# Optimization experiments

Measured on AMD Instinct MI355X. Metric: run time of the kernel, lower is better.

Reference implementation:

```python
import jax, jax.numpy as jnp
import numpy as np

DIM = 1024
NUM_HEADS = 16
NUM_KV_HEADS = 2
HEAD_DIM = DIM // NUM_HEADS          # 64
REPEATS = NUM_HEADS // NUM_KV_HEADS  # 8
WINDOW = 256
HALF = WINDOW // 2                   # 128
BATCH, SEQ = 2, 2048


def setup_inputs() -> dict:
    key = jax.random.key(0)
    ks = jax.random.split(key, 9)
    sc = 1.0 / np.sqrt(DIM)
    return {
        "x":  jax.random.normal(ks[0], (BATCH, SEQ, DIM), jnp.float32),
        "Wq": jax.random.normal(ks[1], (DIM, NUM_HEADS * HEAD_DIM), jnp.float32) * sc,
        "bq": jax.random.normal(ks[2], (NUM_HEADS * HEAD_DIM,), jnp.float32) * 0.01,
        "Wk": jax.random.normal(ks[3], (DIM, NUM_KV_HEADS * HEAD_DIM), jnp.float32) * sc,
        "bk": jax.random.normal(ks[4], (NUM_KV_HEADS * HEAD_DIM,), jnp.float32) * 0.01,
        "Wv": jax.random.normal(ks[5], (DIM, NUM_KV_HEADS * HEAD_DIM), jnp.float32) * sc,
        "bv": jax.random.normal(ks[6], (NUM_KV_HEADS * HEAD_DIM,), jnp.float32) * 0.01,
        "Wo": jax.random.normal(ks[7], (DIM, DIM), jnp.float32) * sc,
        "bo": jax.random.normal(ks[8], (DIM,), jnp.float32) * 0.01,
    }


def reference(x, Wq, bq, Wk, bk, Wv, bv, Wo, bo):
    # Training-path GQA sliding-window attention (faithful to the torch module):
    #  - K/V zero-padded by HALF on each side of the sequence; window of size
    #    WINDOW centered on each query position (unfold with step 1).
    #  - NOTE (faithful): the original code builds mask = tril(ones)[-1], which is
    #    an all-ones row, so masked_fill is a no-op -> NO causal mask inside the
    #    window; padded positions contribute score 0 (not -inf) to the softmax.
    #  - NOTE (faithful): the training path does NOT scale scores by 1/sqrt(d).
    b, s, _ = x.shape
    q = (x @ Wq + bq).reshape(b, s, NUM_HEADS, HEAD_DIM).transpose(0, 2, 1, 3)      # [b,H,s,d]
    k = (x @ Wk + bk).reshape(b, s, NUM_KV_HEADS, HEAD_DIM).transpose(0, 2, 1, 3)   # [b,G,s,d]
    v = (x @ Wv + bv).reshape(b, s, NUM_KV_HEADS, HEAD_DIM).transpose(0, 2, 1, 3)

    kp = jnp.pad(k, ((0, 0), (0, 0), (HALF, HALF), (0, 0)))  # [b,G,s+W,d]
    vp = jnp.pad(v, ((0, 0), (0, 0), (HALF, HALF), (0, 0)))

    # window gather indices: window i covers padded positions [i, i+W)
    idx = jnp.arange(s)[:, None] + jnp.arange(WINDOW)[None, :]  # [s,W]
    k_win = kp[:, :, idx]  # [b,G,s,W,d]  (gather at kv-head granularity, not H)
    v_win = vp[:, :, idx]

    # group query heads by kv head: head h -> kv group h // REPEATS
    qg = q.reshape(b, NUM_KV_HEADS, REPEATS, s, HEAD_DIM)        # [b,G,r,s,d]
    scores = jnp.einsum('bgrsd,bgswd->bgrsw', qg, k_win)         # no scaling (faithful)
    probs = jax.nn.softmax(scores, axis=-1)
    out = jnp.einsum('bgrsw,bgswd->bgrsd', probs, v_win)         # [b,G,r,s,d]

    out = out.reshape(b, NUM_HEADS, s, HEAD_DIM).transpose(0, 2, 1, 3).reshape(b, s, DIM)
    return out @ Wo + bo
```

## Files before the change

kernel.cpp:

```cpp
#include <hip/hip_runtime.h>
#include <hip/hip_fp16.h>

typedef _Float16 h16;
typedef __attribute__((ext_vector_type(4))) _Float16 h16x4;
typedef __attribute__((ext_vector_type(8))) _Float16 h16x8;
typedef __attribute__((ext_vector_type(4))) float f32x4;

#define DIM   1024
#define SEQ   2048
#define NKV   2
#define HD    64
#define HALFW 128
#define NQKV  1280
#define KSTG  288
#define KCOLS 272
#define VSTR  312
#define LOG2E 1.4426950408889634f

__global__ void preprocess_kernel(const float* __restrict__ x,
                                  const float* __restrict__ bq,
                                  const float* __restrict__ bk,
                                  const float* __restrict__ bv,
                                  const float* __restrict__ Wq,
                                  const float* __restrict__ Wk,
                                  const float* __restrict__ Wv,
                                  const float* __restrict__ Wo,
                                  h16* __restrict__ xh, float* __restrict__ bqkv,
                                  h16* __restrict__ wqkvt, h16* __restrict__ wot)
{
    __shared__ float tile[32][33];
    const int tid = threadIdx.x;
    const int blk = blockIdx.x;
    if (blk < 2048) {
        int i = blk * 256 + tid;
        size_t base = (size_t)i * 8;
        float4 a = *(const float4*)(x + base);
        float4 b = *(const float4*)(x + base + 4);
        h16x8 o = { (h16)a.x,(h16)a.y,(h16)a.z,(h16)a.w,
                    (h16)b.x,(h16)b.y,(h16)b.z,(h16)b.w };
        *(h16x8*)(xh + base) = o;
        if (i < NQKV) {
            float v = (i < DIM) ? bq[i] * LOG2E
                                : (i < DIM+128 ? bk[i-DIM] : bv[i-DIM-128]);
            bqkv[i] = v;
        }
        return;
    }
    const int tx = tid & 31, ty = tid >> 5;
    if (blk < 2048 + 1280) {
        int bid = blk - 2048;
        int n0 = (bid % 40) * 32, k0 = (bid / 40) * 32;
        const float* src; int ldn, noff; float scl;
        if (n0 < DIM)          { src = Wq; ldn = DIM; noff = n0; scl = LOG2E; }
        else if (n0 < DIM+128) { src = Wk; ldn = 128; noff = n0 - DIM; scl = 1.f; }
        else                   { src = Wv; ldn = 128; noff = n0 - DIM - 128; scl = 1.f; }
#pragma unroll
        for (int i = 0; i < 4; ++i)
            tile[ty + 8*i][tx] = src[(size_t)(k0 + ty + 8*i)*ldn + noff + tx] * scl;
        __syncthreads();
#pragma unroll
        for (int i = 0; i < 4; ++i)
            wqkvt[(size_t)(n0 + ty + 8*i)*DIM + k0 + tx] = (h16)tile[tx][ty + 8*i];
    } else {
        int bid = blk - 3328;
        int n0 = (bid % 32) * 32, k0 = (bid / 32) * 32;
#pragma unroll
        for (int i = 0; i < 4; ++i)
            tile[ty + 8*i][tx] = Wo[(size_t)(k0 + ty + 8*i)*DIM + n0 + tx];
        __syncthreads();
#pragma unroll
        for (int i = 0; i < 4; ++i)
            wot[(size_t)(n0 + ty + 8*i)*DIM + k0 + tx] = (h16)tile[tx][ty + 8*i];
    }
}

__global__ void vtrans_kernel(const h16* __restrict__ v, h16* __restrict__ vt)
{
    __shared__ h16 tile[32][33];
    const int s0 = blockIdx.x * 32, d0 = blockIdx.y * 32, bg = blockIdx.z;
    const h16* src = v  + (size_t)bg * SEQ * HD;
    h16*       dst = vt + (size_t)bg * SEQ * HD;
    const int tx = threadIdx.x & 31, ty = threadIdx.x >> 5;
#pragma unroll
    for (int i = 0; i < 4; ++i)
        tile[ty + 8*i][tx] = src[(size_t)(s0 + ty + 8*i)*HD + d0 + tx];
    __syncthreads();
#pragma unroll
    for (int i = 0; i < 4; ++i)
        dst[(size_t)(d0 + ty + 8*i)*SEQ + s0 + tx] = tile[tx][ty + 8*i];
}

template<int MODE>
__global__ __launch_bounds__(256, 3)
void gemm_kernel(const h16* __restrict__ A, const h16* __restrict__ Bt,
                 const float* __restrict__ bias,
                 h16* __restrict__ qo, h16* __restrict__ ko, h16* __restrict__ vo,
                 float* __restrict__ co, int K, int nx)
{
    __shared__ __align__(16) h16 As[2][128*64];
    __shared__ __align__(16) h16 Bs[2][64*64];
    const int nwg = gridDim.x, bid = blockIdx.x;
    const int wg = (bid & 7) * (nwg >> 3) + (bid >> 3);
    const int m0 = (wg / nx) * 128, n0 = (wg % nx) * 64;
    const int tid = threadIdx.x, lane = tid & 63, wid = tid >> 6;
    const int wr = wid >> 1, wc = wid & 1;
    f32x4 acc[4][2] = {};

    auto stage = [&](int buf, int kk) {
#pragma unroll
        for (int i = 0; i < 4; ++i) {
            int slot = i*256 + tid;
            int row = slot >> 3;
            int scol = ((slot & 7) ^ (row & 7)) * 8;
            __builtin_amdgcn_global_load_lds(
                (const __attribute__((address_space(1))) void*)(A + (size_t)(m0 + row)*K + kk + scol),
                (__attribute__((address_space(3))) void*)(&As[buf][slot*8]), 16, 0, 0);
        }
#pragma unroll
        for (int i = 0; i < 2; ++i) {
            int slot = i*256 + tid;
            int row = slot >> 3;
            int scol = ((slot & 7) ^ (row & 7)) * 8;
            __builtin_amdgcn_global_load_lds(
                (const __attribute__((address_space(1))) void*)(Bt + (size_t)(n0 + row)*K + kk + scol),
                (__attribute__((address_space(3))) void*)(&Bs[buf][slot*8]), 16, 0, 0);
        }
    };
    auto compute = [&](int buf) {
#pragma unroll
        for (int k2 = 0; k2 < 2; ++k2) {
            h16x8 a[4], b[2];
#pragma unroll
            for (int mi = 0; mi < 4; ++mi) {
                int row = wr*64 + mi*16 + (lane & 15);
                int cc = (k2*4 + (lane >> 4)) ^ (row & 7);
                a[mi] = *(const h16x8*)(&As[buf][row*64 + cc*8]);
            }
#pragma unroll
            for (int ni = 0; ni < 2; ++ni) {
                int row = wc*32 + ni*16 + (lane & 15);
                int cc = (k2*4 + (lane >> 4)) ^ (row & 7);
                b[ni] = *(const h16x8*)(&Bs[buf][row*64 + cc*8]);
            }
#pragma unroll
            for (int mi = 0; mi < 4; ++mi)
#pragma unroll
                for (int ni = 0; ni < 2; ++ni)
                    acc[mi][ni] = __builtin_amdgcn_mfma_f32_16x16x32_f16(a[mi], b[ni], acc[mi][ni], 0, 0, 0);
        }
    };

    const int ns = K >> 6;
    stage(0, 0);
    int cur = 0;
    for (int i = 0; i < ns; ++i) {
        if (i < ns-1) {
            stage(cur ^ 1, (i+1) << 6);
            asm volatile("s_waitcnt vmcnt(6)" ::: "memory");
        } else {
            asm volatile("s_waitcnt vmcnt(0)" ::: "memory");
        }
        __builtin_amdgcn_s_barrier();
        __builtin_amdgcn_sched_barrier(0);
        compute(cur);
        if (i < ns-1) {
            __builtin_amdgcn_s_barrier();
            __builtin_amdgcn_sched_barrier(0);
        }
        cur ^= 1;
    }

#pragma unroll
    for (int ni = 0; ni < 2; ++ni) {
        int n = n0 + wc*32 + ni*16 + (lane & 15);
        float bv = bias[n];
#pragma unroll
        for (int mi = 0; mi < 4; ++mi) {
            int mb = m0 + wr*64 + mi*16 + (lane >> 4)*4;
#pragma unroll
            for (int r = 0; r < 4; ++r) {
                int m = mb + r;
                float v = acc[mi][ni][r] + bv;
                if (MODE == 1) {
                    co[(size_t)m*DIM + n] = v;
                } else {
                    h16 hv = (h16)v;
                    if (n < DIM) {
                        qo[(size_t)m*DIM + n] = hv;
                    } else {
                        int nn = n - DIM;
                        int bi2 = m >> 11, s = m & 2047;
                        int g = (nn & 127) >> 6, d = nn & 63;
                        h16* dstp = (nn < 128) ? ko : vo;
                        dstp[(((size_t)(bi2*NKV + g))*SEQ + s)*HD + d] = hv;
                    }
                }
            }
        }
    }
}

__global__ __launch_bounds__(512)
void attn_kernel(const h16* __restrict__ qb, const h16* __restrict__ kb,
                 const h16* __restrict__ vtb, h16* __restrict__ ob)
{
    extern __shared__ char smem[];
    h16* Ks  = (h16*)smem;
    h16* Vts = (h16*)(smem + 36864);
    h16* Ps  = (h16*)(smem + 36864 + 39936);
    const int tid = threadIdx.x, lane = tid & 63, wid = tid >> 6;
    const int qt = blockIdx.x, g = blockIdx.y, bi = blockIdx.z;
    const int s0 = qt * 32;
    const size_t kvbase = ((size_t)(bi*NKV + g)) * SEQ * HD;

    for (int slot = tid; slot < KSTG*8; slot += 512) {
        int row = slot >> 3, cc = slot & 7;
        int kpos = s0 - HALFW + row;
        h16x8 val = {0,0,0,0,0,0,0,0};
        if (kpos >= 0 && kpos < SEQ)
            val = *(const h16x8*)(kb + kvbase + (size_t)kpos*HD + cc*8);
        *(h16x8*)(Ks + row*64 + ((cc ^ (row & 7)) * 8)) = val;
    }
    for (int slot = tid; slot < 64*38; slot += 512) {
        int row = slot / 38, cc = slot - row*38;
        int c0 = cc * 8;
        int kp0 = s0 - HALFW + c0;
        const h16* vrow = vtb + kvbase + (size_t)row*SEQ;
        h16x8 val = {0,0,0,0,0,0,0,0};
        if (kp0 >= 0 && kp0 + 8 <= SEQ) {
            val = *(const h16x8*)(vrow + kp0);
        } else {
#pragma unroll
            for (int j = 0; j < 8; ++j) {
                int kp = kp0 + j;
                val[j] = (kp >= 0 && kp < SEQ) ? vrow[kp] : (h16)0;
            }
        }
        *(h16x8*)(Vts + row*VSTR + c0) = val;
    }
    h16* P = Ps + wid * 16 * VSTR;
    for (int i = lane; i < 256; i += 64)
        P[(i >> 4)*VSTR + KCOLS + (i & 15)] = (h16)0;
    __syncthreads();

    const int h = g*8 + wid;
    const int colbase = lane & 15;
    const int rowbase = (lane >> 4) * 4;
    const int kg = rowbase;

    for (int strip = 0; strip < 2; ++strip) {
        const int ss0 = s0 + strip*16;
        h16x8 aq[2];
#pragma unroll
        for (int c = 0; c < 2; ++c)
            aq[c] = *(const h16x8*)(qb + ((size_t)(bi*SEQ + ss0 + colbase))*DIM
                                    + h*HD + c*32 + (lane >> 4)*8);

        f32x4 sc[17];
        __builtin_amdgcn_s_setprio(1);
#pragma unroll
        for (int t = 0; t < 17; ++t) {
            f32x4 z = {0.f,0.f,0.f,0.f};
#pragma unroll
            for (int c = 0; c < 2; ++c) {
                int key = strip*16 + t*16 + colbase;
                h16x8 kf = *(const h16x8*)(Ks + key*64 + (((c*4 + (lane >> 4)) ^ (key & 7)) * 8));
                z = __builtin_amdgcn_mfma_f32_16x16x32_f16(kf, aq[c], z, 0, 0, 0);
            }
            sc[t] = z;
        }
        __builtin_amdgcn_s_setprio(0);

        float mx = -1e30f;
#pragma unroll
        for (int r = 0; r < 4; ++r) {
            float v0  = (kg + r >= colbase) ? sc[0][r]  : -1e30f;
            float v16 = (kg + r <  colbase) ? sc[16][r] : -1e30f;
            sc[0][r] = v0; sc[16][r] = v16;
            mx = fmaxf(mx, fmaxf(v0, v16));
        }
#pragma unroll
        for (int t = 1; t < 16; ++t)
#pragma unroll
            for (int r = 0; r < 4; ++r) mx = fmaxf(mx, sc[t][r]);
        mx = fmaxf(mx, __shfl_xor(mx, 16));
        mx = fmaxf(mx, __shfl_xor(mx, 32));
        float sum = 0.f;
#pragma unroll
        for (int t = 0; t < 17; ++t)
#pragma unroll
            for (int r = 0; r < 4; ++r) {
                float p = exp2f(sc[t][r] - mx);
                sc[t][r] = p;
                sum += p;
            }
        sum += __shfl_xor(sum, 16);
        sum += __shfl_xor(sum, 32);
        float inv = 1.0f / sum;

#pragma unroll
        for (int t = 0; t < 17; ++t) {
            h16x4 pk = { (h16)(sc[t][0]*inv), (h16)(sc[t][1]*inv),
                         (h16)(sc[t][2]*inv), (h16)(sc[t][3]*inv) };
            *(h16x4*)(P + colbase*VSTR + t*16 + kg) = pk;
        }

        f32x4 ao[4] = {};
        __builtin_amdgcn_s_setprio(1);
#pragma unroll
        for (int c = 0; c < 9; ++c) {
            h16x8 pa = *(const h16x8*)(P + colbase*VSTR + c*32 + (lane >> 4)*8);
            int vcol = strip*16 + c*32 + (lane >> 4)*8;
#pragma unroll
            for (int t2 = 0; t2 < 4; ++t2) {
                h16x8 vb = *(const h16x8*)(Vts + (t2*16 + colbase)*VSTR + vcol);
                ao[t2] = __builtin_amdgcn_mfma_f32_16x16x32_f16(pa, vb, ao[t2], 0, 0, 0);
            }
        }
        __builtin_amdgcn_s_setprio(0);
#pragma unroll
        for (int t2 = 0; t2 < 4; ++t2)
#pragma unroll
            for (int r = 0; r < 4; ++r)
                ob[((size_t)(bi*SEQ + ss0 + rowbase + r))*DIM + h*HD + t2*16 + colbase]
                    = (h16)ao[t2][r];
        if (strip == 0) __syncthreads();
    }
}

extern "C" void kernel_launch(void* const* d_in, const int* in_sizes, int n_in,
                              void* d_out, int out_size, void* d_ws, size_t ws_size,
                              hipStream_t stream)
{
    const float* x  = (const float*)d_in[0];
    const float* Wq = (const float*)d_in[1];
    const float* bq = (const float*)d_in[2];
    const float* Wk = (const float*)d_in[3];
    const float* bk = (const float*)d_in[4];
    const float* Wv = (const float*)d_in[5];
    const float* bv = (const float*)d_in[6];
    const float* Wo = (const float*)d_in[7];
    const float* bo = (const float*)d_in[8];
    float* out = (float*)d_out;
    char* ws = (char*)d_ws;

    h16*   xh    = (h16*)(ws);
    h16*   wqkvt = (h16*)(ws + 8388608);
    h16*   wot   = (h16*)(ws + 11010048);
    float* bqkv  = (float*)(ws + 13107200);
    h16*   q_b   = (h16*)(ws + 13112320);
    h16*   k_b   = (h16*)(ws + 21500928);
    h16*   vt_b  = (h16*)(ws + 22549504);
    h16*   att_b = (h16*)(ws + 23598080);
    h16*   v_b   = att_b;

    preprocess_kernel<<<4352, 256, 0, stream>>>(x, bq, bk, bv, Wq, Wk, Wv, Wo,
                                                xh, bqkv, wqkvt, wot);
    gemm_kernel<0><<<640, 256, 0, stream>>>(xh, wqkvt, bqkv,
                                            q_b, k_b, v_b, nullptr, DIM, 20);
    vtrans_kernel<<<dim3(64, 2, 4), 256, 0, stream>>>(v_b, vt_b);
    hipFuncSetAttribute((const void*)attn_kernel,
                        hipFuncAttributeMaxDynamicSharedMemorySize, 156672);
    attn_kernel<<<dim3(64,2,2), 512, 156672, stream>>>(q_b, k_b, vt_b, att_b);
    gemm_kernel<1><<<512, 256, 0, stream>>>(att_b, wot, bo,
                                            nullptr, nullptr, nullptr, out, DIM, 16);
}
```

Measured before the change: 68.37 us.

## Read K/V directly from zero-padded global buffers instead of staging in LDS

K and transposed V are written into global buffers padded by HALF zero rows/columns on each side, with the padding zeroed by extra preprocess blocks. The attention kernel then drops LDS staging of K/V and the block-wide barrier, and loads MFMA operands straight from global/L2, keeping only the per-wave P tile in shared memory. Blocks shrink to 256 threads (4 heads each) with a 4-blocks-per-CU launch bound, for more occupancy and less LDS. The cost is that the 8 heads sharing a KV group (now split across two blocks) each issue their own global loads, which depend on cache hits.

After: 92.01 us. 1.35x slower.

```diff
diff --git a/kernel.cpp b/kernel.cpp
--- a/kernel.cpp
+++ b/kernel.cpp
@@ -12,9 +12,9 @@
 #define HD    64
 #define HALFW 128
 #define NQKV  1280
-#define KSTG  288
-#define KCOLS 272
-#define VSTR  312
+#define SPAD  2304
+#define KPS   (SPAD*HD)
+#define PSTR  296
 #define LOG2E 1.4426950408889634f
 
 __global__ void preprocess_kernel(const float* __restrict__ x,
@@ -26,7 +26,8 @@
                                   const float* __restrict__ Wv,
                                   const float* __restrict__ Wo,
                                   h16* __restrict__ xh, float* __restrict__ bqkv,
-                                  h16* __restrict__ wqkvt, h16* __restrict__ wot)
+                                  h16* __restrict__ wqkvt, h16* __restrict__ wot,
+                                  h16* __restrict__ kpad, h16* __restrict__ vtpad)
 {
     __shared__ float tile[32][33];
     const int tid = threadIdx.x;
@@ -46,6 +47,22 @@
         }
         return;
     }
+    if (blk >= 4352) {
+        int idx = (blk - 4352) * 256 + tid;
+        h16x8 z8 = {};
+        if (idx < 8192) {
+            int bg = idx >> 11, j = idx & 2047;
+            size_t off = (j < 1024) ? (size_t)j*8 : (size_t)2176*HD + (size_t)(j-1024)*8;
+            *(h16x8*)(kpad + (size_t)bg*KPS + off) = z8;
+        } else {
+            int i2 = idx - 8192;
+            int bg = i2 >> 11, j = i2 & 2047;
+            int d = j >> 5, r = j & 31;
+            size_t off = (size_t)d*SPAD + ((r & 16) ? 2176 : 0) + (size_t)(r & 15)*8;
+            *(h16x8*)(vtpad + (size_t)bg*KPS + off) = z8;
+        }
+        return;
+    }
     const int tx = tid & 31, ty = tid >> 5;
     if (blk < 2048 + 1280) {
         int bid = blk - 2048;
@@ -79,7 +96,7 @@
     __shared__ h16 tile[32][33];
     const int s0 = blockIdx.x * 32, d0 = blockIdx.y * 32, bg = blockIdx.z;
     const h16* src = v  + (size_t)bg * SEQ * HD;
-    h16*       dst = vt + (size_t)bg * SEQ * HD;
+    h16*       dst = vt + (size_t)bg * KPS;
     const int tx = threadIdx.x & 31, ty = threadIdx.x >> 5;
 #pragma unroll
     for (int i = 0; i < 4; ++i)
@@ -87,7 +104,7 @@
     __syncthreads();
 #pragma unroll
     for (int i = 0; i < 4; ++i)
-        dst[(size_t)(d0 + ty + 8*i)*SEQ + s0 + tx] = tile[tx][ty + 8*i];
+        dst[(size_t)(d0 + ty + 8*i)*SPAD + HALFW + s0 + tx] = tile[tx][ty + 8*i];
 }
 
 template<int MODE>
@@ -191,8 +208,10 @@
                         int nn = n - DIM;
                         int bi2 = m >> 11, s = m & 2047;
                         int g = (nn & 127) >> 6, d = nn & 63;
-                        h16* dstp = (nn < 128) ? ko : vo;
-                        dstp[(((size_t)(bi2*NKV + g))*SEQ + s)*HD + d] = hv;
+                        if (nn < 128)
+                            ko[((size_t)(bi2*NKV + g)*SPAD + s + HALFW)*HD + d] = hv;
+                        else
+                            vo[(((size_t)(bi2*NKV + g))*SEQ + s)*HD + d] = hv;
                     }
                 }
             }
@@ -200,61 +219,31 @@
     }
 }
 
-__global__ __launch_bounds__(512)
-void attn_kernel(const h16* __restrict__ qb, const h16* __restrict__ kb,
-                 const h16* __restrict__ vtb, h16* __restrict__ ob)
-{
-    extern __shared__ char smem[];
-    h16* Ks  = (h16*)smem;
-    h16* Vts = (h16*)(smem + 36864);
-    h16* Ps  = (h16*)(smem + 36864 + 39936);
+__global__ __launch_bounds__(256, 4)
+void attn_kernel(const h16* __restrict__ qb, const h16* __restrict__ kpad,
+                 const h16* __restrict__ vtpad, h16* __restrict__ ob)
+{
+    __shared__ h16 Ps[4][16][PSTR];
     const int tid = threadIdx.x, lane = tid & 63, wid = tid >> 6;
-    const int qt = blockIdx.x, g = blockIdx.y, bi = blockIdx.z;
+    const int qt = blockIdx.x, quad = blockIdx.y, bi = blockIdx.z;
+    const int g = quad >> 1, h = quad*4 + wid;
     const int s0 = qt * 32;
-    const size_t kvbase = ((size_t)(bi*NKV + g)) * SEQ * HD;
-
-    for (int slot = tid; slot < KSTG*8; slot += 512) {
-        int row = slot >> 3, cc = slot & 7;
-        int kpos = s0 - HALFW + row;
-        h16x8 val = {0,0,0,0,0,0,0,0};
-        if (kpos >= 0 && kpos < SEQ)
-            val = *(const h16x8*)(kb + kvbase + (size_t)kpos*HD + cc*8);
-        *(h16x8*)(Ks + row*64 + ((cc ^ (row & 7)) * 8)) = val;
-    }
-    for (int slot = tid; slot < 64*38; slot += 512) {
-        int row = slot / 38, cc = slot - row*38;
-        int c0 = cc * 8;
-        int kp0 = s0 - HALFW + c0;
-        const h16* vrow = vtb + kvbase + (size_t)row*SEQ;
-        h16x8 val = {0,0,0,0,0,0,0,0};
-        if (kp0 >= 0 && kp0 + 8 <= SEQ) {
-            val = *(const h16x8*)(vrow + kp0);
-        } else {
-#pragma unroll
-            for (int j = 0; j < 8; ++j) {
-                int kp = kp0 + j;
-                val[j] = (kp >= 0 && kp < SEQ) ? vrow[kp] : (h16)0;
-            }
-        }
-        *(h16x8*)(Vts + row*VSTR + c0) = val;
-    }
-    h16* P = Ps + wid * 16 * VSTR;
+    const int q = lane & 15, hi = lane >> 4;
+    const int rowbase = hi * 4;
+    const h16* Kb = kpad  + (size_t)(bi*NKV + g)*KPS + (size_t)s0*HD;
+    const h16* Vb = vtpad + (size_t)(bi*NKV + g)*KPS + s0;
+    h16* P = &Ps[wid][0][0];
+
     for (int i = lane; i < 256; i += 64)
-        P[(i >> 4)*VSTR + KCOLS + (i & 15)] = (h16)0;
-    __syncthreads();
-
-    const int h = g*8 + wid;
-    const int colbase = lane & 15;
-    const int rowbase = (lane >> 4) * 4;
-    const int kg = rowbase;
+        P[(i >> 4)*PSTR + 272 + (i & 15)] = (h16)0;
 
     for (int strip = 0; strip < 2; ++strip) {
         const int ss0 = s0 + strip*16;
         h16x8 aq[2];
 #pragma unroll
         for (int c = 0; c < 2; ++c)
-            aq[c] = *(const h16x8*)(qb + ((size_t)(bi*SEQ + ss0 + colbase))*DIM
-                                    + h*HD + c*32 + (lane >> 4)*8);
+            aq[c] = *(const h16x8*)(qb + ((size_t)(bi*SEQ + ss0 + q))*DIM
+                                    + h*HD + c*32 + hi*8);
 
         f32x4 sc[17];
         __builtin_amdgcn_s_setprio(1);
@@ -263,8 +252,8 @@
             f32x4 z = {0.f,0.f,0.f,0.f};
 #pragma unroll
             for (int c = 0; c < 2; ++c) {
-                int key = strip*16 + t*16 + colbase;
-                h16x8 kf = *(const h16x8*)(Ks + key*64 + (((c*4 + (lane >> 4)) ^ (key & 7)) * 8));
+                h16x8 kf = *(const h16x8*)(Kb + (size_t)(strip*16 + t*16 + q)*HD
+                                           + (c*4 + hi)*8);
                 z = __builtin_amdgcn_mfma_f32_16x16x32_f16(kf, aq[c], z, 0, 0, 0);
             }
             sc[t] = z;
@@ -274,8 +263,8 @@
         float mx = -1e30f;
 #pragma unroll
         for (int r = 0; r < 4; ++r) {
-            float v0  = (kg + r >= colbase) ? sc[0][r]  : -1e30f;
-            float v16 = (kg + r <  colbase) ? sc[16][r] : -1e30f;
+            float v0  = (rowbase + r >= q) ? sc[0][r]  : -1e30f;
+            float v16 = (rowbase + r <  q) ? sc[16][r] : -1e30f;
             sc[0][r] = v0; sc[16][r] = v16;
             mx = fmaxf(mx, fmaxf(v0, v16));
         }
@@ -302,18 +291,18 @@
         for (int t = 0; t < 17; ++t) {
             h16x4 pk = { (h16)(sc[t][0]*inv), (h16)(sc[t][1]*inv),
                          (h16)(sc[t][2]*inv), (h16)(sc[t][3]*inv) };
-            *(h16x4*)(P + colbase*VSTR + t*16 + kg) = pk;
+            *(h16x4*)(P + q*PSTR + t*16 + rowbase) = pk;
         }
 
         f32x4 ao[4] = {};
         __builtin_amdgcn_s_setprio(1);
 #pragma unroll
         for (int c = 0; c < 9; ++c) {
-            h16x8 pa = *(const h16x8*)(P + colbase*VSTR + c*32 + (lane >> 4)*8);
-            int vcol = strip*16 + c*32 + (lane >> 4)*8;
+            h16x8 pa = *(const h16x8*)(P + q*PSTR + c*32 + hi*8);
+            int vcol = strip*16 + c*32 + hi*8;
 #pragma unroll
             for (int t2 = 0; t2 < 4; ++t2) {
-                h16x8 vb = *(const h16x8*)(Vts + (t2*16 + colbase)*VSTR + vcol);
+                h16x8 vb = *(const h16x8*)(Vb + (size_t)(t2*16 + q)*SPAD + vcol);
                 ao[t2] = __builtin_amdgcn_mfma_f32_16x16x32_f16(pa, vb, ao[t2], 0, 0, 0);
             }
         }
@@ -322,9 +311,8 @@
         for (int t2 = 0; t2 < 4; ++t2)
 #pragma unroll
             for (int r = 0; r < 4; ++r)
-                ob[((size_t)(bi*SEQ + ss0 + rowbase + r))*DIM + h*HD + t2*16 + colbase]
+                ob[((size_t)(bi*SEQ + ss0 + rowbase + r))*DIM + h*HD + t2*16 + q]
                     = (h16)ao[t2][r];
-        if (strip == 0) __syncthreads();
     }
 }
 
@@ -349,19 +337,17 @@
     h16*   wot   = (h16*)(ws + 11010048);
     float* bqkv  = (float*)(ws + 13107200);
     h16*   q_b   = (h16*)(ws + 13112320);
-    h16*   k_b   = (h16*)(ws + 21500928);
-    h16*   vt_b  = (h16*)(ws + 22549504);
-    h16*   att_b = (h16*)(ws + 23598080);
+    h16*   k_pad = (h16*)(ws + 21500928);
+    h16*   vt_pad= (h16*)(ws + 22680576);
+    h16*   att_b = (h16*)(ws + 23860224);
     h16*   v_b   = att_b;
 
-    preprocess_kernel<<<4352, 256, 0, stream>>>(x, bq, bk, bv, Wq, Wk, Wv, Wo,
-                                                xh, bqkv, wqkvt, wot);
+    preprocess_kernel<<<4416, 256, 0, stream>>>(x, bq, bk, bv, Wq, Wk, Wv, Wo,
+                                                xh, bqkv, wqkvt, wot, k_pad, vt_pad);
     gemm_kernel<0><<<640, 256, 0, stream>>>(xh, wqkvt, bqkv,
-                                            q_b, k_b, v_b, nullptr, DIM, 20);
-    vtrans_kernel<<<dim3(64, 2, 4), 256, 0, stream>>>(v_b, vt_b);
-    hipFuncSetAttribute((const void*)attn_kernel,
-                        hipFuncAttributeMaxDynamicSharedMemorySize, 156672);
-    attn_kernel<<<dim3(64,2,2), 512, 156672, stream>>>(q_b, k_b, vt_b, att_b);
+                                            q_b, k_pad, v_b, nullptr, DIM, 20);
+    vtrans_kernel<<<dim3(64, 2, 4), 256, 0, stream>>>(v_b, vt_pad);
+    attn_kernel<<<dim3(64, 4, 2), 256, 0, stream>>>(q_b, k_pad, vt_pad, att_b);
     gemm_kernel<1><<<512, 256, 0, stream>>>(att_b, wot, bo,
                                             nullptr, nullptr, nullptr, out, DIM, 16);
 }
```
